# Optimization experiments

Measured on AMD Instinct MI355X. Metric: run time of the kernel, lower is better.

The kernel has to match this reference:

```python
import jax, jax.numpy as jnp
import numpy as np

MANIFOLD_DIM = 256
EPS = 1e-8

def quaternion_normalize(q):
    # q: (..., 4) -> unit quaternions
    return q / (jnp.linalg.norm(q, axis=-1, keepdims=True) + EPS)

def quaternion_mul(a, b):
    # Hamilton product, broadcasting over leading dims. a, b: (..., 4)
    aw, ax, ay, az = a[..., 0], a[..., 1], a[..., 2], a[..., 3]
    bw, bx, by, bz = b[..., 0], b[..., 1], b[..., 2], b[..., 3]
    return jnp.stack([
        aw * bw - ax * bx - ay * by - az * bz,
        aw * bx + ax * bw + ay * bz - az * by,
        aw * by - ax * bz + ay * bw + az * bx,
        aw * bz + ax * by - ay * bx + az * bw,
    ], axis=-1)

def compute_berry_phase(path):
    # path: (B, N, 4). gamma = 2*acos(Re(q0*q1*...*q_{N-1}*q0))
    path = quaternion_normalize(path)
    # ordered product via log-depth parallel scan (quaternion mul is associative)
    prod_all = jax.lax.associative_scan(quaternion_mul, path, axis=1)[:, -1]  # (B, 4)
    prod = quaternion_mul(prod_all, path[:, 0])
    return 2.0 * jnp.arccos(jnp.clip(prod[..., 0], -1.0, 1.0))  # (B,)

def holomorphic_audit(q_state):
    # torch.gradient(t)[0] == gradient along dim 0 (batch axis), unit spacing.
    # dw+dx+dy+dz == gradient of the component-sum (linearity of gradient).
    df = jnp.abs(jnp.gradient(q_state.sum(axis=-1), axis=0))  # (B, N)
    res = jnp.mean(df)
    return res < 0.05, res

def _to_quaternion(x):
    B = x.shape[0]
    return x.reshape(B, -1, 4)

def setup_inputs() -> dict:
    key = jax.random.key(0)
    ks = jax.random.split(key, 9)
    B, HW, L, G, D = 8, 4096, 8192, 4096, MANIFOLD_DIM
    s = 0.05  # keep latents small so Berry product stays numerically tame
    return {
        "vision_data": jax.random.normal(ks[0], (B, HW, 3), jnp.float32),
        "text_data": jax.random.normal(ks[1], (B, L, 1), jnp.float32),
        "genomic_data": jax.random.normal(ks[2], (B, G, 4), jnp.float32),
        "Wv": jax.random.normal(ks[3], (3, D), jnp.float32) * s,
        "bv": jax.random.normal(ks[4], (D,), jnp.float32) * s,
        "Wt": jax.random.normal(ks[5], (1, D), jnp.float32) * s,
        "bt": jax.random.normal(ks[6], (D,), jnp.float32) * s,
        "Wg": jax.random.normal(ks[7], (4, D), jnp.float32) * s,
        "bg": jax.random.normal(ks[8], (D,), jnp.float32) * s,
    }

def reference(vision_data, text_data, genomic_data, Wv, bv, Wt, bt, Wg, bg):
    v_lat = vision_data @ Wv + bv      # (B, HW, 256)
    t_lat = text_data @ Wt + bt        # (B, L, 256)
    g_lat = genomic_data @ Wg + bg     # (B, G, 256)
    v_path = _to_quaternion(v_lat)     # (B, HW*64, 4)
    t_path = _to_quaternion(t_lat)
    g_path = _to_quaternion(g_lat)
    phi_v = compute_berry_phase(v_path)
    phi_t = compute_berry_phase(t_path)
    phi_g = compute_berry_phase(g_path)
    interference = jnp.abs(phi_v.mean() - phi_t.mean())
    genomic_invariant_score = jnp.exp(-jnp.abs(phi_g - interference))  # (B,)
    _, res_v = holomorphic_audit(v_path)
    _, res_t = holomorphic_audit(t_path)
    return genomic_invariant_score, interference, res_v, res_t
```

## Files before the change

kernel.cpp:

```cpp
#include <hip/hip_runtime.h>
#include <math.h>

#define BB 8
#define HW 4096
#define LTXT 8192
#define GG 4096
#define DD 256


struct QF { float w, x, y, z; };

__device__ __forceinline__ QF qmulf(const QF a, const QF b) {
    QF r;
    r.w = fmaf(a.w, b.w, -fmaf(a.x, b.x, fmaf(a.y, b.y, a.z * b.z)));
    r.x = fmaf(a.w, b.x, fmaf(a.x, b.w, fmaf(a.y, b.z, -(a.z * b.y))));
    r.y = fmaf(a.w, b.y, fmaf(a.y, b.w, fmaf(a.z, b.x, -(a.x * b.z))));
    r.z = fmaf(a.w, b.z, fmaf(a.x, b.y, fmaf(a.z, b.w, -(a.y * b.x))));
    return r;
}

__device__ __forceinline__ QF wave_ordered_prod(QF p, int lane) {
    #pragma unroll
    for (int s = 1; s < 64; s <<= 1) {
        QF o;
        o.w = __shfl_xor(p.w, s, 64);
        o.x = __shfl_xor(p.x, s, 64);
        o.y = __shfl_xor(p.y, s, 64);
        o.z = __shfl_xor(p.z, s, 64);
        const bool hi = (lane & s) != 0;
        QF a = hi ? o : p;
        QF b = hi ? p : o;
        p = qmulf(a, b);
    }
    return p;
}

template<int K, int BQ>
__device__ __forceinline__ void chain_block(
    const float* __restrict__ X, const float* __restrict__ W,
    const float* __restrict__ bias, int rowBase,
    float* __restrict__ out4, float* sprod)
{
    constexpr int V = K + 1;
    constexpr int NB = 64 / BQ;
    const int t = threadIdx.x;
    const int r = rowBase + t;
    float xv[K];
    #pragma unroll
    for (int k = 0; k < K; ++k) xv[k] = X[(size_t)r * K + k];

    float4 A[BQ * V], Bb[BQ * V];
    QF p = {1.0f, 0.0f, 0.0f, 0.0f};

    auto LOADB = [&](float4* dst, int bidx) {
        const float* bb = bias + 4 * (bidx * BQ);
        const float* wb = W + 4 * (bidx * BQ);
        #pragma unroll
        for (int j = 0; j < BQ; ++j) {
            dst[j * V + 0] = *(const float4*)(bb + 4 * j);
            #pragma unroll
            for (int k = 0; k < K; ++k)
                dst[j * V + 1 + k] = *(const float4*)(wb + k * DD + 4 * j);
        }
    };

    auto COMPUTE = [&](const float4* src, int bidx) {
        QF pb; float tt, rr;
        #pragma unroll
        for (int j = 0; j < BQ; ++j) {
            const float4 b4 = src[j * V + 0];
            float l0 = b4.x, l1 = b4.y, l2 = b4.z, l3 = b4.w;
            #pragma unroll
            for (int k = 0; k < K; ++k) {
                const float4 w4 = src[j * V + 1 + k];
                l0 = fmaf(xv[k], w4.x, l0);
                l1 = fmaf(xv[k], w4.y, l1);
                l2 = fmaf(xv[k], w4.z, l2);
                l3 = fmaf(xv[k], w4.w, l3);
            }
            const float n2 = fmaf(l0, l0, fmaf(l1, l1, fmaf(l2, l2, l3 * l3)));
            QF q = { l0, l1, l2, l3 };
            if (j == 0) { pb = q; tt = n2; rr = __builtin_amdgcn_rsqf(n2); }
            else {
                pb = qmulf(pb, q);
                tt *= n2;
                rr += __builtin_amdgcn_rsqf(n2);
            }
        }
        const float S  = sqrtf(tt) * fmaf(1e-8f, rr, 1.0f);
        const float inv = 1.0f / S;
        QF pbn = { pb.w * inv, pb.x * inv, pb.y * inv, pb.z * inv };
        if (bidx == 0) p = pbn;
        else           p = qmulf(p, pbn);
    };

    LOADB(A, 0);
    for (int gg = 0; gg < NB / 2; ++gg) {
        LOADB(Bb, 2 * gg + 1);
        COMPUTE(A, 2 * gg);
        const int nb = (2 * gg + 2 < NB) ? (2 * gg + 2) : (NB - 1);
        LOADB(A, nb);
        COMPUTE(Bb, 2 * gg + 1);
    }

    const int lane = t & 63;
    p = wave_ordered_prod(p, lane);

    const int w = t >> 6;
    if (lane == 0) { sprod[w*4+0] = p.w; sprod[w*4+1] = p.x; sprod[w*4+2] = p.y; sprod[w*4+3] = p.z; }
    __syncthreads();
    if (t == 0) {
        QF pp = { sprod[0], sprod[1], sprod[2], sprod[3] };
        #pragma unroll
        for (int wv = 1; wv < 4; ++wv) {
            QF o = { sprod[wv*4+0], sprod[wv*4+1], sprod[wv*4+2], sprod[wv*4+3] };
            pp = qmulf(pp, o);
        }
        float4 outv = { pp.w, pp.x, pp.y, pp.z };
        *(float4*)out4 = outv;
    }
}

__global__ __launch_bounds__(256) void worker_kernel(
    const float* __restrict__ vis, const float* __restrict__ txt, const float* __restrict__ gen,
    const float* __restrict__ Wv, const float* __restrict__ bv,
    const float* __restrict__ Wt, const float* __restrict__ bt,
    const float* __restrict__ Wg, const float* __restrict__ bg,
    float* __restrict__ wsf, double* __restrict__ dws)
{
    __shared__ double sred[256];
    float* sprod = (float*)sred;

    const int t  = threadIdx.x;
    const int id = blockIdx.x;

    if (id < 128) {
        const int b = id >> 4, chunk = id & 15;
        chain_block<3, 4>(vis + (size_t)b * HW * 3, Wv, bv, chunk * 256,
                          wsf + (size_t)id * 4, sprod);
    } else if (id < 384) {
        const int i2 = id - 128;
        const int b = i2 >> 5, chunk = i2 & 31;
        chain_block<1, 8>(txt + (size_t)b * LTXT, Wt, bt, chunk * 256,
                          wsf + 512 + (size_t)i2 * 4, sprod);
    } else if (id < 512) {
        const int i2 = id - 384;
        const int b = i2 >> 4, chunk = i2 & 15;
        chain_block<4, 2>(gen + (size_t)b * GG * 4, Wg, bg, chunk * 256,
                          wsf + 1536 + (size_t)i2 * 4, sprod);
    } else if (id < 528) {
        const int aid = id - 512;
        const int r = aid * 256 + t;
        float gx[8], gy[8], gz[8];
        {
            float vx[8], vy[8], vz[8];
            #pragma unroll
            for (int b = 0; b < 8; ++b) {
                const size_t base = ((size_t)b * HW + r) * 3;
                vx[b] = vis[base]; vy[b] = vis[base+1]; vz[b] = vis[base+2];
            }
            #pragma unroll
            for (int b = 0; b < 8; ++b) {
                if (b == 0)      { gx[b] = vx[1]-vx[0];  gy[b] = vy[1]-vy[0];  gz[b] = vz[1]-vz[0]; }
                else if (b == 7) { gx[b] = vx[7]-vx[6];  gy[b] = vy[7]-vy[6];  gz[b] = vz[7]-vz[6]; }
                else             { gx[b] = (vx[b+1]-vx[b-1])*0.5f; gy[b] = (vy[b+1]-vy[b-1])*0.5f; gz[b] = (vz[b+1]-vz[b-1])*0.5f; }
            }
        }
        double acc = 0.0;
        #pragma unroll 4
        for (int i = 0; i < 64; ++i) {
            const float4 a0 = *(const float4*)(Wv + 4*i);
            const float4 a1 = *(const float4*)(Wv + DD + 4*i);
            const float4 a2 = *(const float4*)(Wv + 2*DD + 4*i);
            const float wq0 = a0.x + a0.y + a0.z + a0.w;
            const float wq1 = a1.x + a1.y + a1.z + a1.w;
            const float wq2 = a2.x + a2.y + a2.z + a2.w;
            float acc8 = 0.0f;
            #pragma unroll
            for (int b = 0; b < 8; ++b)
                acc8 += fabsf(fmaf(gx[b], wq0, fmaf(gy[b], wq1, gz[b] * wq2)));
            acc += (double)acc8;
        }
        sred[t] = acc;
        __syncthreads();
        for (int off = 128; off > 0; off >>= 1) {
            if (t < off) sred[t] += sred[t + off];
            __syncthreads();
        }
        if (t == 0) dws[aid] = sred[0];
    } else {
        const int aid = id - 528;
        const int l = aid * 256 + t;
        float tv[8];
        #pragma unroll
        for (int b = 0; b < 8; ++b) tv[b] = txt[(size_t)b * LTXT + l];
        double acc = 0.0;
        #pragma unroll
        for (int b = 0; b < 8; ++b) {
            float gb;
            if (b == 0)      gb = tv[1] - tv[0];
            else if (b == 7) gb = tv[7] - tv[6];
            else             gb = (tv[b+1] - tv[b-1]) * 0.5f;
            acc += (double)fabsf(gb);
        }
        sred[t] = acc;
        __syncthreads();
        for (int off = 128; off > 0; off >>= 1) {
            if (t < off) sred[t] += sred[t + off];
            __syncthreads();
        }
        if (t == 0) dws[16 + aid] = sred[0];
    }
}

__global__ __launch_bounds__(256) void finalize_kernel(
    const float* __restrict__ vis, const float* __restrict__ txt, const float* __restrict__ gen,
    const float* __restrict__ Wv, const float* __restrict__ bv,
    const float* __restrict__ Wt, const float* __restrict__ bt,
    const float* __restrict__ Wg, const float* __restrict__ bg,
    const float* __restrict__ wsf, const double* __restrict__ dws,
    float* __restrict__ out)
{
    __shared__ float sphi[24];
    __shared__ double sred[256];
    __shared__ double s_sumv, s_sumt, s_sumw;
    const int t = threadIdx.x;
    const int lane = t & 63, w = t >> 6;

    #pragma unroll
    for (int j = 0; j < 6; ++j) {
        const int pair = w * 6 + j;
        const int m = pair >> 3, b = pair & 7;
        const int nch = (m == 1) ? 32 : 16;
        const float* base = wsf + ((m == 0) ? 0 : (m == 1) ? 512 : 1536) + (size_t)b * nch * 4;
        QF p = { 1.0f, 0.0f, 0.0f, 0.0f };
        if (lane < nch) {
            const float4 c0 = *(const float4*)(base + lane * 4);
            p = { c0.x, c0.y, c0.z, c0.w };
        }
        p = wave_ordered_prod(p, lane);
        if (lane == 0) {
            float lat[4];
            if (m == 0) {
                const float x0 = vis[(size_t)b*HW*3], x1 = vis[(size_t)b*HW*3+1], x2 = vis[(size_t)b*HW*3+2];
                #pragma unroll
                for (int c = 0; c < 4; ++c)
                    lat[c] = fmaf(x0, Wv[c], fmaf(x1, Wv[DD+c], fmaf(x2, Wv[2*DD+c], bv[c])));
            } else if (m == 1) {
                const float x0 = txt[(size_t)b*LTXT];
                #pragma unroll
                for (int c = 0; c < 4; ++c) lat[c] = fmaf(x0, Wt[c], bt[c]);
            } else {
                const float x0 = gen[(size_t)b*GG*4], x1 = gen[(size_t)b*GG*4+1],
                            x2 = gen[(size_t)b*GG*4+2], x3 = gen[(size_t)b*GG*4+3];
                #pragma unroll
                for (int c = 0; c < 4; ++c)
                    lat[c] = fmaf(x0, Wg[c], fmaf(x1, Wg[DD+c], fmaf(x2, Wg[2*DD+c], fmaf(x3, Wg[3*DD+c], bg[c]))));
            }
            const float n = sqrtf(fmaf(lat[0], lat[0], fmaf(lat[1], lat[1], fmaf(lat[2], lat[2], lat[3] * lat[3]))));
            const float inv = 1.0f / (n + 1e-8f);
            QF q0 = { lat[0]*inv, lat[1]*inv, lat[2]*inv, lat[3]*inv };
            p = qmulf(p, q0);
            float ww = p.w;
            ww = fminf(1.0f, fmaxf(-1.0f, ww));
            sphi[pair] = 2.0f * acosf(ww);
        }
    }
    __syncthreads();

    sred[t] = (t < 16) ? dws[t] : 0.0; __syncthreads();
    for (int off = 128; off > 0; off >>= 1) { if (t < off) sred[t] += sred[t+off]; __syncthreads(); }
    if (t == 0) s_sumv = sred[0];
    __syncthreads();

    sred[t] = (t < 32) ? dws[16 + t] : 0.0; __syncthreads();
    for (int off = 128; off > 0; off >>= 1) { if (t < off) sred[t] += sred[t+off]; __syncthreads(); }
    if (t == 0) s_sumt = sred[0];
    __syncthreads();

    double aw = 0.0;
    if (t < 64) {
        const int d0 = 4 * t;
        aw = (double)fabsf(Wt[d0] + Wt[d0+1] + Wt[d0+2] + Wt[d0+3]);
    }
    sred[t] = aw; __syncthreads();
    for (int off = 128; off > 0; off >>= 1) { if (t < off) sred[t] += sred[t+off]; __syncthreads(); }
    if (t == 0) s_sumw = sred[0];
    __syncthreads();

    if (t == 0) {
        float mv = 0.0f, mt = 0.0f;
        for (int b = 0; b < 8; ++b) { mv += sphi[b]; mt += sphi[8 + b]; }
        mv *= 0.125f; mt *= 0.125f;
        const float interf = fabsf(mv - mt);
        for (int b = 0; b < 8; ++b)
            out[b] = expf(-fabsf(sphi[16 + b] - interf));
        out[8]  = interf;
        out[9]  = (float)(s_sumv / 2097152.0);
        out[10] = (float)(s_sumt * s_sumw / 4194304.0);
    }
}

extern "C" void kernel_launch(void* const* d_in, const int* in_sizes, int n_in,
                              void* d_out, int out_size, void* d_ws, size_t ws_size,
                              hipStream_t stream) {
    (void)in_sizes; (void)n_in; (void)out_size; (void)ws_size;
    const float* vis = (const float*)d_in[0];
    const float* txt = (const float*)d_in[1];
    const float* gen = (const float*)d_in[2];
    const float* Wv  = (const float*)d_in[3];
    const float* bv  = (const float*)d_in[4];
    const float* Wt  = (const float*)d_in[5];
    const float* bt  = (const float*)d_in[6];
    const float* Wg  = (const float*)d_in[7];
    const float* bg  = (const float*)d_in[8];
    float*  wsf = (float*)d_ws;
    double* dws = (double*)((char*)d_ws + 65536);
    float*  out = (float*)d_out;

    hipLaunchKernelGGL(worker_kernel, dim3(560), dim3(256), 0, stream,
                       vis, txt, gen, Wv, bv, Wt, bt, Wg, bg, wsf, dws);
    hipLaunchKernelGGL(finalize_kernel, dim3(1), dim3(256), 0, stream,
                       vis, txt, gen, Wv, bv, Wt, bt, Wg, bg, wsf, dws, out);
}
```

Before: 33.28 us.

## Process two rows per thread with packed float2 FMA quaternion chains

Each thread now computes two rows (t and t+128) at once, using 2-wide vector FMAs that can map to packed FP32 instructions. Blocks shrink to 128 threads, so the chain grid keeps the same block count while the audit blocks double. Per-block normalisation changes from a sqrt and divide to an exponent-based power-of-two rescale, with one true normalisation at the end. This cuts per-element instruction count and transcendental use, at the cost of higher register pressure, fewer threads for latency hiding, and a changed block-reduction order in which the two halves are combined in thread 0.

```diff
diff --git a/kernel.cpp b/kernel.cpp
--- a/kernel.cpp
+++ b/kernel.cpp
@@ -8,7 +8,13 @@
 #define DD 256
 
 
+typedef float v2f __attribute__((ext_vector_type(2)));
+#define VFMA __builtin_elementwise_fma
+
+__device__ __forceinline__ v2f vsplat(float s) { v2f r; r.x = s; r.y = s; return r; }
+
 struct QF { float w, x, y, z; };
+struct QP { v2f w, x, y, z; };
 
 __device__ __forceinline__ QF qmulf(const QF a, const QF b) {
     QF r;
@@ -16,6 +22,15 @@
     r.x = fmaf(a.w, b.x, fmaf(a.x, b.w, fmaf(a.y, b.z, -(a.z * b.y))));
     r.y = fmaf(a.w, b.y, fmaf(a.y, b.w, fmaf(a.z, b.x, -(a.x * b.z))));
     r.z = fmaf(a.w, b.z, fmaf(a.x, b.y, fmaf(a.z, b.w, -(a.y * b.x))));
+    return r;
+}
+
+__device__ __forceinline__ QP qmulp(const QP a, const QP b) {
+    QP r;
+    r.w = VFMA(a.w, b.w, -VFMA(a.x, b.x, VFMA(a.y, b.y, a.z * b.z)));
+    r.x = VFMA(a.w, b.x, VFMA(a.x, b.w, VFMA(a.y, b.z, -(a.z * b.y))));
+    r.y = VFMA(a.w, b.y, VFMA(a.y, b.w, VFMA(a.z, b.x, -(a.x * b.z))));
+    r.z = VFMA(a.w, b.z, VFMA(a.x, b.y, VFMA(a.z, b.w, -(a.y * b.x))));
     return r;
 }
 
@@ -35,8 +50,25 @@
     return p;
 }
 
+__device__ __forceinline__ QP wave_ordered_prod_p(QP p, int lane) {
+    #pragma unroll
+    for (int s = 1; s < 64; s <<= 1) {
+        QP o;
+        o.w.x = __shfl_xor(p.w.x, s, 64); o.w.y = __shfl_xor(p.w.y, s, 64);
+        o.x.x = __shfl_xor(p.x.x, s, 64); o.x.y = __shfl_xor(p.x.y, s, 64);
+        o.y.x = __shfl_xor(p.y.x, s, 64); o.y.y = __shfl_xor(p.y.y, s, 64);
+        o.z.x = __shfl_xor(p.z.x, s, 64); o.z.y = __shfl_xor(p.z.y, s, 64);
+        const bool hi = (lane & s) != 0;
+        QP a, b;
+        a.w = hi ? o.w : p.w; a.x = hi ? o.x : p.x; a.y = hi ? o.y : p.y; a.z = hi ? o.z : p.z;
+        b.w = hi ? p.w : o.w; b.x = hi ? p.x : o.x; b.y = hi ? p.y : o.y; b.z = hi ? p.z : o.z;
+        p = qmulp(a, b);
+    }
+    return p;
+}
+
 template<int K, int BQ>
-__device__ __forceinline__ void chain_block(
+__device__ __forceinline__ void chain_pair(
     const float* __restrict__ X, const float* __restrict__ W,
     const float* __restrict__ bias, int rowBase,
     float* __restrict__ out4, float* sprod)
@@ -44,13 +76,19 @@
     constexpr int V = K + 1;
     constexpr int NB = 64 / BQ;
     const int t = threadIdx.x;
-    const int r = rowBase + t;
-    float xv[K];
+    const int rA = rowBase + t;
+    const int rB = rA + 128;
+
+    v2f xv[K];
     #pragma unroll
-    for (int k = 0; k < K; ++k) xv[k] = X[(size_t)r * K + k];
+    for (int k = 0; k < K; ++k) {
+        xv[k].x = X[(size_t)rA * K + k];
+        xv[k].y = X[(size_t)rB * K + k];
+    }
 
     float4 A[BQ * V], Bb[BQ * V];
-    QF p = {1.0f, 0.0f, 0.0f, 0.0f};
+    QP p;
+    float MA = 1.0f, MB = 1.0f, rrA = 0.0f, rrB = 0.0f;
 
     auto LOADB = [&](float4* dst, int bidx) {
         const float* bb = bias + 4 * (bidx * BQ);
@@ -65,33 +103,36 @@
     };
 
     auto COMPUTE = [&](const float4* src, int bidx) {
-        QF pb; float tt, rr;
+        QP pb; v2f tt;
         #pragma unroll
         for (int j = 0; j < BQ; ++j) {
             const float4 b4 = src[j * V + 0];
-            float l0 = b4.x, l1 = b4.y, l2 = b4.z, l3 = b4.w;
+            v2f l0 = vsplat(b4.x), l1 = vsplat(b4.y), l2 = vsplat(b4.z), l3 = vsplat(b4.w);
             #pragma unroll
             for (int k = 0; k < K; ++k) {
                 const float4 w4 = src[j * V + 1 + k];
-                l0 = fmaf(xv[k], w4.x, l0);
-                l1 = fmaf(xv[k], w4.y, l1);
-                l2 = fmaf(xv[k], w4.z, l2);
-                l3 = fmaf(xv[k], w4.w, l3);
+                l0 = VFMA(xv[k], vsplat(w4.x), l0);
+                l1 = VFMA(xv[k], vsplat(w4.y), l1);
+                l2 = VFMA(xv[k], vsplat(w4.z), l2);
+                l3 = VFMA(xv[k], vsplat(w4.w), l3);
             }
-            const float n2 = fmaf(l0, l0, fmaf(l1, l1, fmaf(l2, l2, l3 * l3)));
-            QF q = { l0, l1, l2, l3 };
-            if (j == 0) { pb = q; tt = n2; rr = __builtin_amdgcn_rsqf(n2); }
-            else {
-                pb = qmulf(pb, q);
-                tt *= n2;
-                rr += __builtin_amdgcn_rsqf(n2);
-            }
-        }
-        const float S  = sqrtf(tt) * fmaf(1e-8f, rr, 1.0f);
-        const float inv = 1.0f / S;
-        QF pbn = { pb.w * inv, pb.x * inv, pb.y * inv, pb.z * inv };
-        if (bidx == 0) p = pbn;
-        else           p = qmulf(p, pbn);
+            const v2f n2 = VFMA(l0, l0, VFMA(l1, l1, VFMA(l2, l2, l3 * l3)));
+            rrA += __builtin_amdgcn_rsqf(n2.x);
+            rrB += __builtin_amdgcn_rsqf(n2.y);
+            QP q; q.w = l0; q.x = l1; q.y = l2; q.z = l3;
+            if (j == 0) { pb = q; tt = n2; }
+            else        { pb = qmulp(pb, q); tt *= n2; }
+        }
+        const int e2A = ((__float_as_int(tt.x) >> 23) - 127) >> 1;
+        const int e2B = ((__float_as_int(tt.y) >> 23) - 127) >> 1;
+        const float scA = __int_as_float((127 - e2A) << 23);
+        const float scB = __int_as_float((127 - e2B) << 23);
+        MA *= tt.x * (scA * scA);
+        MB *= tt.y * (scB * scB);
+        v2f sc; sc.x = scA; sc.y = scB;
+        pb.w *= sc; pb.x *= sc; pb.y *= sc; pb.z *= sc;
+        if (bidx == 0) p = pb;
+        else           p = qmulp(p, pb);
     };
 
     LOADB(A, 0);
@@ -103,32 +144,42 @@
         COMPUTE(Bb, 2 * gg + 1);
     }
 
+    {
+        const float invA = 1.0f / (sqrtf(MA) * fmaf(1e-8f, rrA, 1.0f));
+        const float invB = 1.0f / (sqrtf(MB) * fmaf(1e-8f, rrB, 1.0f));
+        v2f iv; iv.x = invA; iv.y = invB;
+        p.w *= iv; p.x *= iv; p.y *= iv; p.z *= iv;
+    }
+
     const int lane = t & 63;
-    p = wave_ordered_prod(p, lane);
+    p = wave_ordered_prod_p(p, lane);
 
     const int w = t >> 6;
-    if (lane == 0) { sprod[w*4+0] = p.w; sprod[w*4+1] = p.x; sprod[w*4+2] = p.y; sprod[w*4+3] = p.z; }
+    if (lane == 0) {
+        float* s8 = sprod + w * 8;
+        s8[0] = p.w.x; s8[1] = p.x.x; s8[2] = p.y.x; s8[3] = p.z.x;
+        s8[4] = p.w.y; s8[5] = p.x.y; s8[6] = p.y.y; s8[7] = p.z.y;
+    }
     __syncthreads();
     if (t == 0) {
-        QF pp = { sprod[0], sprod[1], sprod[2], sprod[3] };
-        #pragma unroll
-        for (int wv = 1; wv < 4; ++wv) {
-            QF o = { sprod[wv*4+0], sprod[wv*4+1], sprod[wv*4+2], sprod[wv*4+3] };
-            pp = qmulf(pp, o);
-        }
-        float4 outv = { pp.w, pp.x, pp.y, pp.z };
+        QF A0 = { sprod[0], sprod[1], sprod[2], sprod[3] };
+        QF A1 = { sprod[8], sprod[9], sprod[10], sprod[11] };
+        QF B0 = { sprod[4], sprod[5], sprod[6], sprod[7] };
+        QF B1 = { sprod[12], sprod[13], sprod[14], sprod[15] };
+        QF r = qmulf(qmulf(qmulf(A0, A1), B0), B1);
+        float4 outv = { r.w, r.x, r.y, r.z };
         *(float4*)out4 = outv;
     }
 }
 
-__global__ __launch_bounds__(256) void worker_kernel(
+__global__ __launch_bounds__(128) void worker_kernel(
     const float* __restrict__ vis, const float* __restrict__ txt, const float* __restrict__ gen,
     const float* __restrict__ Wv, const float* __restrict__ bv,
     const float* __restrict__ Wt, const float* __restrict__ bt,
     const float* __restrict__ Wg, const float* __restrict__ bg,
     float* __restrict__ wsf, double* __restrict__ dws)
 {
-    __shared__ double sred[256];
+    __shared__ double sred[128];
     float* sprod = (float*)sred;
 
     const int t  = threadIdx.x;
@@ -136,21 +187,21 @@
 
     if (id < 128) {
         const int b = id >> 4, chunk = id & 15;
-        chain_block<3, 4>(vis + (size_t)b * HW * 3, Wv, bv, chunk * 256,
-                          wsf + (size_t)id * 4, sprod);
+        chain_pair<3, 4>(vis + (size_t)b * HW * 3, Wv, bv, chunk * 256,
+                         wsf + (size_t)id * 4, sprod);
     } else if (id < 384) {
         const int i2 = id - 128;
         const int b = i2 >> 5, chunk = i2 & 31;
-        chain_block<1, 8>(txt + (size_t)b * LTXT, Wt, bt, chunk * 256,
-                          wsf + 512 + (size_t)i2 * 4, sprod);
+        chain_pair<1, 4>(txt + (size_t)b * LTXT, Wt, bt, chunk * 256,
+                         wsf + 512 + (size_t)i2 * 4, sprod);
     } else if (id < 512) {
         const int i2 = id - 384;
         const int b = i2 >> 4, chunk = i2 & 15;
-        chain_block<4, 2>(gen + (size_t)b * GG * 4, Wg, bg, chunk * 256,
-                          wsf + 1536 + (size_t)i2 * 4, sprod);
-    } else if (id < 528) {
+        chain_pair<4, 2>(gen + (size_t)b * GG * 4, Wg, bg, chunk * 256,
+                         wsf + 1536 + (size_t)i2 * 4, sprod);
+    } else if (id < 544) {
         const int aid = id - 512;
-        const int r = aid * 256 + t;
+        const int r = aid * 128 + t;
         float gx[8], gy[8], gz[8];
         {
             float vx[8], vy[8], vz[8];
@@ -183,14 +234,14 @@
         }
         sred[t] = acc;
         __syncthreads();
-        for (int off = 128; off > 0; off >>= 1) {
+        for (int off = 64; off > 0; off >>= 1) {
             if (t < off) sred[t] += sred[t + off];
             __syncthreads();
         }
         if (t == 0) dws[aid] = sred[0];
     } else {
-        const int aid = id - 528;
-        const int l = aid * 256 + t;
+        const int aid = id - 544;
+        const int l = aid * 128 + t;
         float tv[8];
         #pragma unroll
         for (int b = 0; b < 8; ++b) tv[b] = txt[(size_t)b * LTXT + l];
@@ -205,11 +256,11 @@
         }
         sred[t] = acc;
         __syncthreads();
-        for (int off = 128; off > 0; off >>= 1) {
+        for (int off = 64; off > 0; off >>= 1) {
             if (t < off) sred[t] += sred[t + off];
             __syncthreads();
         }
-        if (t == 0) dws[16 + aid] = sred[0];
+        if (t == 0) dws[32 + aid] = sred[0];
     }
 }
 
@@ -268,12 +319,12 @@
     }
     __syncthreads();
 
-    sred[t] = (t < 16) ? dws[t] : 0.0; __syncthreads();
+    sred[t] = (t < 32) ? dws[t] : 0.0; __syncthreads();
     for (int off = 128; off > 0; off >>= 1) { if (t < off) sred[t] += sred[t+off]; __syncthreads(); }
     if (t == 0) s_sumv = sred[0];
     __syncthreads();
 
-    sred[t] = (t < 32) ? dws[16 + t] : 0.0; __syncthreads();
+    sred[t] = (t < 64) ? dws[32 + t] : 0.0; __syncthreads();
     for (int off = 128; off > 0; off >>= 1) { if (t < off) sred[t] += sred[t+off]; __syncthreads(); }
     if (t == 0) s_sumt = sred[0];
     __syncthreads();
@@ -318,7 +369,7 @@
     double* dws = (double*)((char*)d_ws + 65536);
     float*  out = (float*)d_out;
 
-    hipLaunchKernelGGL(worker_kernel, dim3(560), dim3(256), 0, stream,
+    hipLaunchKernelGGL(worker_kernel, dim3(608), dim3(128), 0, stream,
                        vis, txt, gen, Wv, bv, Wt, bt, Wg, bg, wsf, dws);
     hipLaunchKernelGGL(finalize_kernel, dim3(1), dim3(256), 0, stream,
                        vis, txt, gen, Wv, bv, Wt, bt, Wg, bg, wsf, dws, out);
```

Result: faster. 30.43 us (median of 2 runs) (-8.6%).
